# Kernel optimization log

Hardware: AMD Instinct MI355X
Metric: run time of the kernel (lower is better)

The kernel has to match this reference:

```python
import jax, jax.numpy as jnp
import numpy as np

D_MODEL, D_K, D_V, H = 512, 64, 64, 8
B, NQ, NK = 4, 2048, 2048


def setup_inputs() -> dict:
    key = jax.random.key(0)
    ks = jax.random.split(key, 14)
    s = 0.02
    return {
        "queries": jax.random.normal(ks[0], (B, NQ, D_MODEL), jnp.float32),
        "keys": jax.random.normal(ks[1], (B, NK, D_MODEL), jnp.float32),
        "values": jax.random.normal(ks[2], (B, NK, D_MODEL), jnp.float32),
        "attention_weights": jax.random.uniform(ks[3], (B, H, NQ, NK), jnp.float32),
        "attention_mask": jax.random.bernoulli(ks[4], 0.1, (B, H, NQ, NK)),
        "Wq": jax.random.normal(ks[5], (D_MODEL, H * D_K), jnp.float32) * s,
        "bq": jnp.zeros((H * D_K,), jnp.float32),
        "Wk": jax.random.normal(ks[6], (D_MODEL, H * D_K), jnp.float32) * s,
        "bk": jnp.zeros((H * D_K,), jnp.float32),
        "Wv": jax.random.normal(ks[7], (D_MODEL, H * D_V), jnp.float32) * s,
        "bv": jnp.zeros((H * D_V,), jnp.float32),
        "Wo": jax.random.normal(ks[8], (H * D_V, D_MODEL), jnp.float32) * s,
        "bo": jnp.zeros((D_MODEL,), jnp.float32),
    }


def reference(queries, keys, values, attention_weights, attention_mask,
              Wq, bq, Wk, bk, Wv, bv, Wo, bo):
    b_s, nq, _ = queries.shape
    nk = keys.shape[1]
    # projections -> (b, h, seq, d)
    q = (queries @ Wq + bq).reshape(b_s, nq, H, D_K).transpose(0, 2, 1, 3)
    k = (keys @ Wk + bk).reshape(b_s, nk, H, D_K).transpose(0, 2, 1, 3)
    v = (values @ Wv + bv).reshape(b_s, nk, H, D_V).transpose(0, 2, 1, 3)
    scale = 1.0 / np.sqrt(D_K).astype(np.float32)
    att = jnp.einsum("bhqd,bhkd->bhqk", q, k) * scale
    att = att * attention_weights
    att = jnp.where(attention_mask, -jnp.inf, att)
    att = jax.nn.softmax(att, axis=-1)
    out = jnp.einsum("bhqk,bhkd->bhqd", att, v)
    out = out.transpose(0, 2, 1, 3).reshape(b_s, nq, H * D_V)
    return out @ Wo + bo
```

## Files before the change

### kernel.cpp

```cpp
#include <hip/hip_runtime.h>
#include <hip/hip_bf16.h>
#include <math.h>

#define B_   4
#define H_   8
#define NQ_  2048
#define NK_  2048
#define DM_  512
#define DK_  64
#define WL_  262144

typedef short  bf16x8 __attribute__((ext_vector_type(8)));
typedef float  f32x4  __attribute__((ext_vector_type(4)));

static __device__ __forceinline__ f32x4 MFMA16(bf16x8 a, bf16x8 b, f32x4 c) {
    return __builtin_amdgcn_mfma_f32_16x16x32_bf16(a, b, c, 0, 0, 0);
}
static __device__ __forceinline__ unsigned short f2bf(float f) {
    __hip_bfloat16 h = __float2bfloat16(f);
    unsigned short u; __builtin_memcpy(&u, &h, 2); return u;
}
static __device__ __forceinline__ float bf2f(unsigned short u) {
    unsigned int x = ((unsigned int)u) << 16;
    float f; __builtin_memcpy(&f, &x, 4); return f;
}
static __device__ __forceinline__ void glds16(const void* g, void* l) {
    __builtin_amdgcn_global_load_lds(
        (__attribute__((address_space(1))) const void*)g,
        (__attribute__((address_space(3))) void*)l, 16, 0, 0);
}

__global__ __launch_bounds__(256) void conv_mask(const unsigned char* __restrict__ Mk,
                                                 unsigned long long* __restrict__ bits)
{
    __shared__ int s_flag;
    const int tid = threadIdx.x;
    if (tid == 0) s_flag = 0;
    __syncthreads();
    {
        bool any = false;
#pragma unroll
        for (int i = 1; i < 16; i += 4)
            if (Mk[tid*16 + i]) any = true;
        if (any) s_flag = 1;
    }
    __syncthreads();

    const long long NELEM = (long long)B_*H_*NQ_*NK_;
    const long long nth   = (long long)gridDim.x * 256;
    const long long T     = (long long)blockIdx.x * 256 + tid;
    unsigned short* b16   = (unsigned short*)bits;
    const uint4*    src   = (const uint4*)Mk;

    if (s_flag) {
        const long long n = NELEM / 16;
        for (long long t = T; t < n; t += nth) {
            const uint4 u = src[t];
            const unsigned int w[4] = {u.x, u.y, u.z, u.w};
            unsigned int m = 0;
#pragma unroll
            for (int j = 0; j < 4; ++j)
#pragma unroll
                for (int b2 = 0; b2 < 4; ++b2)
                    if ((w[j] >> (8*b2)) & 0xffu) m |= 1u << (4*j + b2);
            b16[t] = (unsigned short)m;
        }
    } else {
        const long long n = NELEM / 4;
        const int l3 = tid & 3;
        for (long long t = T; t < n; t += nth) {
            const uint4 u = src[t];
            const unsigned int nib = (u.x ? 1u : 0u) | (u.y ? 2u : 0u) |
                                     (u.z ? 4u : 0u) | (u.w ? 8u : 0u);
            unsigned int v = nib << (4*l3);
            v |= __shfl_xor(v, 1, 64);
            v |= __shfl_xor(v, 2, 64);
            if (l3 == 0) b16[t >> 2] = (unsigned short)v;
        }
    }
}

__global__ __launch_bounds__(256) void wprep(const float* __restrict__ Wq,
                                             const float* __restrict__ Wk,
                                             const float* __restrict__ Wv,
                                             const float* __restrict__ Wo,
                                             unsigned short* __restrict__ out)
{
    __shared__ float tile[64][65];
    const int tid = threadIdx.x;
    const int k0 = blockIdx.x * 64, n0 = blockIdx.y * 64, w = blockIdx.z;
    const float* W = (w == 0) ? Wq : (w == 1) ? Wk : (w == 2) ? Wv : Wo;
    unsigned short* WTh = out + (size_t)w * 2 * WL_;
    unsigned short* WTl = WTh + WL_;

#pragma unroll
    for (int rd = 0; rd < 4; ++rd) {
        const int k = (tid >> 4) + 16*rd, c4 = (tid & 15) * 4;
        const float4 v4 = *(const float4*)(W + (size_t)(k0 + k)*DM_ + n0 + c4);
        tile[k][c4+0] = v4.x; tile[k][c4+1] = v4.y;
        tile[k][c4+2] = v4.z; tile[k][c4+3] = v4.w;
    }
    __syncthreads();
#pragma unroll
    for (int rd = 0; rd < 4; ++rd) {
        const int n = (tid >> 4) + 16*rd, kk = (tid & 15) * 4;
        unsigned short hh[4], ll[4];
#pragma unroll
        for (int j = 0; j < 4; ++j) {
            const float f = tile[kk + j][n];
            hh[j] = f2bf(f);
            ll[j] = f2bf(f - bf2f(hh[j]));
        }
        *(ushort4*)(WTh + (size_t)(n0 + n)*DM_ + k0 + kk) = make_ushort4(hh[0],hh[1],hh[2],hh[3]);
        *(ushort4*)(WTl + (size_t)(n0 + n)*DM_ + k0 + kk) = make_ushort4(ll[0],ll[1],ll[2],ll[3]);
    }
}

template<int MODE>
__global__ __launch_bounds__(256) void gemm_split(
    const float* __restrict__ A,
    const unsigned short* __restrict__ WTh,
    const unsigned short* __restrict__ WTl,
    const float* __restrict__ bias,
    void* __restrict__ outv, const float oscale)
{
    __shared__ unsigned short Ah[64][64], Al[64][64], Bh[64][64], Bl[64][64];

    const int tid = threadIdx.x;
    const int w = tid >> 6, lane = tid & 63, g = lane >> 4, r = lane & 15;
    const int m0 = blockIdx.x * 64, n0 = blockIdx.y * 64;

    char* pAh = (char*)&Ah[0][0];
    char* pAl = (char*)&Al[0][0];
    char* pBh = (char*)&Bh[0][0];
    char* pBl = (char*)&Bl[0][0];

    const f32x4 z4 = {0.f, 0.f, 0.f, 0.f};
    f32x4 acc[4] = {z4, z4, z4, z4};

    for (int kt = 0; kt < DM_; kt += 64) {
#pragma unroll
        for (int rd = 0; rd < 4; ++rd) {
            const int row = (tid >> 4) + 16*rd;
            const int c4  = (tid & 15) * 4;
            const float4 a4 = *(const float4*)(A + (size_t)(m0 + row)*DM_ + kt + c4);
            const float av[4] = {a4.x, a4.y, a4.z, a4.w};
            unsigned short hh[4];
#pragma unroll
            for (int j = 0; j < 4; ++j) hh[j] = f2bf(av[j]);
            const int bo = (c4 * 2) ^ ((row & 7) << 4);
            *(ushort4*)(pAh + row*128 + bo) = make_ushort4(hh[0],hh[1],hh[2],hh[3]);
            if (MODE == 2) {
                unsigned short ll[4];
#pragma unroll
                for (int j = 0; j < 4; ++j) ll[j] = f2bf(av[j] - bf2f(hh[j]));
                *(ushort4*)(pAl + row*128 + bo) = make_ushort4(ll[0],ll[1],ll[2],ll[3]);
            }
        }
#pragma unroll
        for (int rd = 0; rd < 2; ++rd) {
            const int idx = tid + 256*rd;
            const int row = idx >> 3;
            const int cb  = (idx & 7) * 16;
            const int bo  = cb ^ ((row & 7) << 4);
            const size_t goff = (size_t)(n0 + row)*DM_ + kt + (cb >> 1);
            *(bf16x8*)(pBh + row*128 + bo) = *(const bf16x8*)(WTh + goff);
            *(bf16x8*)(pBl + row*128 + bo) = *(const bf16x8*)(WTl + goff);
        }
        __syncthreads();

        const int swr = (r & 7) << 4;
#pragma unroll
        for (int ks = 0; ks < 2; ++ks) {
            const int xo = (64*ks + 16*g) ^ swr;
            const bf16x8 xh = *(const bf16x8*)(pAh + (16*w + r)*128 + xo);
#pragma unroll
            for (int nt = 0; nt < 4; ++nt) {
                const bf16x8 bh = *(const bf16x8*)(pBh + (16*nt + r)*128 + xo);
                const bf16x8 bl = *(const bf16x8*)(pBl + (16*nt + r)*128 + xo);
                if (MODE == 1) {
                    acc[nt] = MFMA16(xh, bh, acc[nt]);
                    acc[nt] = MFMA16(xh, bl, acc[nt]);
                } else if (MODE == 0) {
                    acc[nt] = MFMA16(bh, xh, acc[nt]);
                    acc[nt] = MFMA16(bl, xh, acc[nt]);
                } else {
                    const bf16x8 xl = *(const bf16x8*)(pAl + (16*w + r)*128 + xo);
                    acc[nt] = MFMA16(bh, xh, acc[nt]);
                    acc[nt] = MFMA16(bh, xl, acc[nt]);
                    acc[nt] = MFMA16(bl, xh, acc[nt]);
                }
            }
        }
        __syncthreads();
    }

    if (MODE == 0) {
        const int m = m0 + 16*w + r;
        const int b = m >> 11, q = m & 2047, h = blockIdx.y;
        unsigned short* dst = (unsigned short*)outv + (((size_t)(b*H_ + h))*NQ_ + q)*DK_;
#pragma unroll
        for (int nt = 0; nt < 4; ++nt) {
            unsigned short u[4];
#pragma unroll
            for (int j = 0; j < 4; ++j)
                u[j] = f2bf((acc[nt][j] + bias[n0 + 16*nt + 4*g + j]) * oscale);
            *(ushort4*)(dst + 16*nt + 4*g) = make_ushort4(u[0],u[1],u[2],u[3]);
        }
    } else if (MODE == 1) {
        const int b = m0 >> 11, h = blockIdx.y;
        const int key = (m0 & 2047) + 16*w + 4*g;
#pragma unroll
        for (int nt = 0; nt < 4; ++nt) {
            const int dv = 16*nt + r;
            const float bv = bias[n0 + dv];
            unsigned short u[4];
#pragma unroll
            for (int j = 0; j < 4; ++j) u[j] = f2bf(acc[nt][j] + bv);
            *(ushort4*)((unsigned short*)outv +
                        (((size_t)(b*H_ + h))*DK_ + dv)*NK_ + key) = make_ushort4(u[0],u[1],u[2],u[3]);
        }
    } else {
        const int m = m0 + 16*w + r;
        float* dst = (float*)outv + (size_t)m*DM_ + n0;
#pragma unroll
        for (int nt = 0; nt < 4; ++nt) {
            float4 o4;
            o4.x = acc[nt][0] + bias[n0 + 16*nt + 4*g + 0];
            o4.y = acc[nt][1] + bias[n0 + 16*nt + 4*g + 1];
            o4.z = acc[nt][2] + bias[n0 + 16*nt + 4*g + 2];
            o4.w = acc[nt][3] + bias[n0 + 16*nt + 4*g + 3];
            *(float4*)(dst + 16*nt + 4*g) = o4;
        }
    }
}

__global__ __launch_bounds__(256, 2) void attn_mfma(
    const unsigned short* __restrict__ Qb,
    const unsigned short* __restrict__ Kb,
    const unsigned short* __restrict__ Vt,
    const float* __restrict__ Wt,
    const unsigned long long* __restrict__ Mb,
    float* __restrict__ O)
{
    __shared__ unsigned short KT[2][64][64];
    __shared__ unsigned short VTs[2][64][64];
    __shared__ float          WT[2][64][64];
    __shared__ short          Pl[4][1024];

    const int tid  = threadIdx.x;
    const int wv   = tid >> 6, lane = tid & 63;
    const int g    = lane >> 4, r = lane & 15;
    const int q0   = blockIdx.x * 64 + wv * 16;
    const int bh   = blockIdx.y;

    const size_t kvBase = (size_t)bh * NK_ * DK_;
    const unsigned short* qp = Qb + kvBase + (size_t)(q0 + r)*DK_ + 8*g;
    const bf16x8 qf0 = *(const bf16x8*)qp;
    const bf16x8 qf1 = *(const bf16x8*)(qp + 32);

    const float* wblock = Wt + ((size_t)bh*NQ_ + blockIdx.x*64)*NK_;
    const unsigned long long* brow = Mb + ((size_t)bh*NQ_ + q0 + r)*(NK_/64);
    const unsigned short* kg = Kb + kvBase;
    const unsigned short* vg = Vt + kvBase;

    const f32x4 zero4 = {0.f, 0.f, 0.f, 0.f};
    f32x4 oa0 = zero4, oa1 = zero4, oa2 = zero4, oa3 = zero4;
    float m_run = -1e30f, l_run = 0.f;

    char* pbase = (char*)&Pl[wv][0];
    const int roff = r * 128;
    const int sw   = (r & 7) << 4;

    const int kv_soff = 8 * ((lane & 7) ^ (lane >> 3));
    const int kv_r8   = lane >> 3;
    const int w_r4    = lane >> 4;

    auto stage = [&](int pbuf, int i) {
        const int kt = i * 64;
#pragma unroll
        for (int c = 0; c < 2; ++c) {
            const int rowl = 16*wv + c*8 + kv_r8;
            glds16(kg + (size_t)(kt + rowl)*DK_ + kv_soff,
                   &KT[pbuf][16*wv + c*8][0] + lane*8);
            glds16(vg + (size_t)rowl*NK_ + kt + kv_soff,
                   &VTs[pbuf][16*wv + c*8][0] + lane*8);
        }
#pragma unroll
        for (int c = 0; c < 4; ++c) {
            const int rowl = 16*wv + c*4 + w_r4;
            glds16(wblock + (size_t)rowl*NK_ + kt + 4*((lane & 15) ^ (c*4 + w_r4)),
                   &WT[pbuf][16*wv + c*4][0] + lane*4);
        }
    };

    stage(0, 0);
    __syncthreads();

#pragma unroll 1
    for (int i = 0; i < 32; ++i) {
        const int p = i & 1;

        if (i + 1 < 32) stage(p ^ 1, i + 1);
        const unsigned long long bcur = brow[i];

        f32x4 sa0 = zero4, sa1 = zero4, sa2 = zero4, sa3 = zero4;
        {
            const bf16x8 k00 = *(const bf16x8*)&KT[p][ 0 + r][8*((g    ) ^ (r & 7))];
            const bf16x8 k01 = *(const bf16x8*)&KT[p][ 0 + r][8*((g + 4) ^ (r & 7))];
            const bf16x8 k10 = *(const bf16x8*)&KT[p][16 + r][8*((g    ) ^ (r & 7))];
            const bf16x8 k11 = *(const bf16x8*)&KT[p][16 + r][8*((g + 4) ^ (r & 7))];
            const bf16x8 k20 = *(const bf16x8*)&KT[p][32 + r][8*((g    ) ^ (r & 7))];
            const bf16x8 k21 = *(const bf16x8*)&KT[p][32 + r][8*((g + 4) ^ (r & 7))];
            const bf16x8 k30 = *(const bf16x8*)&KT[p][48 + r][8*((g    ) ^ (r & 7))];
            const bf16x8 k31 = *(const bf16x8*)&KT[p][48 + r][8*((g + 4) ^ (r & 7))];
            sa0 = MFMA16(k00, qf0, sa0); sa0 = MFMA16(k01, qf1, sa0);
            sa1 = MFMA16(k10, qf0, sa1); sa1 = MFMA16(k11, qf1, sa1);
            sa2 = MFMA16(k20, qf0, sa2); sa2 = MFMA16(k21, qf1, sa2);
            sa3 = MFMA16(k30, qf0, sa3); sa3 = MFMA16(k31, qf1, sa3);
        }

        f32x4 wf[4];
#pragma unroll
        for (int t = 0; t < 4; ++t)
            wf[t] = *(const f32x4*)&WT[p][16*wv + r][4*((4*t + g) ^ r)];

        float lg[16];
        const f32x4 sav[4] = {sa0, sa1, sa2, sa3};
#pragma unroll
        for (int t = 0; t < 4; ++t) {
            const unsigned int half = (t & 2) ? (unsigned int)(bcur >> 32)
                                              : (unsigned int)bcur;
#pragma unroll
            for (int j = 0; j < 4; ++j) {
                const unsigned int bit = (half >> (16*(t & 1) + 4*g + j)) & 1u;
                lg[4*t+j] = bit ? -1e30f : sav[t][j] * wf[t][j];
            }
        }

        float mx = lg[0];
#pragma unroll
        for (int i2 = 1; i2 < 16; ++i2) mx = fmaxf(mx, lg[i2]);
        mx = fmaxf(mx, __shfl_xor(mx, 16, 64));
        mx = fmaxf(mx, __shfl_xor(mx, 32, 64));
        const float mnew = fmaxf(m_run, mx);
        const float fsc  = __expf(m_run - mnew);
        m_run = mnew;
        float p16[16], rs = 0.f;
#pragma unroll
        for (int i2 = 0; i2 < 16; ++i2) { p16[i2] = __expf(lg[i2] - mnew); rs += p16[i2]; }
        rs += __shfl_xor(rs, 16, 64);
        rs += __shfl_xor(rs, 32, 64);
        l_run = l_run * fsc + rs;

#pragma unroll
        for (int t = 0; t < 4; ++t) {
            const unsigned int w0 = (unsigned int)f2bf(p16[4*t+0]) |
                                    ((unsigned int)f2bf(p16[4*t+1]) << 16);
            const unsigned int w1 = (unsigned int)f2bf(p16[4*t+2]) |
                                    ((unsigned int)f2bf(p16[4*t+3]) << 16);
            *(int2*)(pbase + roff + ((32*t + 8*g) ^ sw)) = make_int2((int)w0, (int)w1);
        }
        const bf16x8 pa0 = *(const bf16x8*)(pbase + roff + ((     16*g) ^ sw));
        const bf16x8 pa1 = *(const bf16x8*)(pbase + roff + ((64 + 16*g) ^ sw));

        float fr[4];
#pragma unroll
        for (int j = 0; j < 4; ++j) fr[j] = __shfl(fsc, 4*g + j, 64);
#pragma unroll
        for (int j = 0; j < 4; ++j) {
            oa0[j] *= fr[j]; oa1[j] *= fr[j]; oa2[j] *= fr[j]; oa3[j] *= fr[j];
        }

        {
            const bf16x8 v00 = *(const bf16x8*)&VTs[p][ 0 + r][8*((g    ) ^ (r & 7))];
            const bf16x8 v01 = *(const bf16x8*)&VTs[p][16 + r][8*((g    ) ^ (r & 7))];
            const bf16x8 v02 = *(const bf16x8*)&VTs[p][32 + r][8*((g    ) ^ (r & 7))];
            const bf16x8 v03 = *(const bf16x8*)&VTs[p][48 + r][8*((g    ) ^ (r & 7))];
            const bf16x8 v10 = *(const bf16x8*)&VTs[p][ 0 + r][8*((g + 4) ^ (r & 7))];
            const bf16x8 v11 = *(const bf16x8*)&VTs[p][16 + r][8*((g + 4) ^ (r & 7))];
            const bf16x8 v12 = *(const bf16x8*)&VTs[p][32 + r][8*((g + 4) ^ (r & 7))];
            const bf16x8 v13 = *(const bf16x8*)&VTs[p][48 + r][8*((g + 4) ^ (r & 7))];
            oa0 = MFMA16(pa0, v00, oa0); oa1 = MFMA16(pa0, v01, oa1);
            oa2 = MFMA16(pa0, v02, oa2); oa3 = MFMA16(pa0, v03, oa3);
            oa0 = MFMA16(pa1, v10, oa0); oa1 = MFMA16(pa1, v11, oa1);
            oa2 = MFMA16(pa1, v12, oa2); oa3 = MFMA16(pa1, v13, oa3);
        }

        __syncthreads();
    }

    const float inv = 1.0f / l_run;
    float ir[4];
#pragma unroll
    for (int j = 0; j < 4; ++j) ir[j] = __shfl(inv, 4*g + j, 64);
    const int bb = bh >> 3, h = bh & 7;
    const f32x4 oav[4] = {oa0, oa1, oa2, oa3};
#pragma unroll
    for (int nt = 0; nt < 4; ++nt)
#pragma unroll
        for (int j = 0; j < 4; ++j)
            O[((size_t)(bb*NQ_ + q0 + 4*g + j))*DM_ + h*64 + 16*nt + r] = oav[nt][j] * ir[j];
}

extern "C" void kernel_launch(void* const* d_in, const int* in_sizes, int n_in,
                              void* d_out, int out_size, void* d_ws, size_t ws_size,
                              hipStream_t stream) {
    (void)in_sizes; (void)n_in; (void)out_size; (void)ws_size;

    const float* q    = (const float*)d_in[0];
    const float* k    = (const float*)d_in[1];
    const float* v    = (const float*)d_in[2];
    const float* attw = (const float*)d_in[3];
    const unsigned char* mask = (const unsigned char*)d_in[4];
    const float* Wq = (const float*)d_in[5];
    const float* bq = (const float*)d_in[6];
    const float* Wk = (const float*)d_in[7];
    const float* bk = (const float*)d_in[8];
    const float* Wv = (const float*)d_in[9];
    const float* bv = (const float*)d_in[10];
    const float* Wo = (const float*)d_in[11];
    const float* bo = (const float*)d_in[12];
    float* out = (float*)d_out;

    const long long NE = (long long)B_*H_*NQ_*DK_;
    unsigned short* q_bf = (unsigned short*)d_ws;
    unsigned short* k_bf = q_bf + NE;
    unsigned short* vT   = q_bf + 2*NE;
    unsigned short* wt   = q_bf + 3*NE;
    unsigned long long* bits = (unsigned long long*)(wt + 8LL*WL_);
    const long long NB = (long long)B_*H_*NQ_*NK_/64;
    float* o_ws = (float*)(bits + NB);

    const dim3 blk(256);
    wprep<<<dim3(8, 8, 4), blk, 0, stream>>>(Wq, Wk, Wv, Wo, wt);
    conv_mask<<<dim3(2048), blk, 0, stream>>>(mask, bits);

    const dim3 gg(128, 8);
    gemm_split<0><<<gg, blk, 0, stream>>>(q, wt + 0*WL_, wt + 1*WL_, bq, q_bf, 0.125f);
    gemm_split<0><<<gg, blk, 0, stream>>>(k, wt + 2*WL_, wt + 3*WL_, bk, k_bf, 1.0f);
    gemm_split<1><<<gg, blk, 0, stream>>>(v, wt + 4*WL_, wt + 5*WL_, bv, vT, 1.0f);

    attn_mfma<<<dim3(NQ_/64, B_*H_), blk, 0, stream>>>(q_bf, k_bf, vT, attw, bits, o_ws);

    gemm_split<2><<<gg, blk, 0, stream>>>(o_ws, wt + 6*WL_, wt + 7*WL_, bo, out, 1.0f);
}
```

Baseline: 405.0 us.

## Halve attention key tile to 32 and raise occupancy to four blocks per CU

The attention kernel now processes 32 keys per iteration instead of 64, which halves the shared-memory K/V/weight staging buffers and the per-thread register arrays. The launch bound is raised from 2 to 4 blocks per CU, and the mask is read as 32-bit words, with staging and swizzle patterns rewritten for the narrower tiles. The goal is more resident waves to hide memory latency on the attention-weight stream. The cost is twice as many loop iterations, online-softmax rescales and __syncthreads barriers, with less work per barrier.

```diff
diff --git a/kernel.cpp b/kernel.cpp
--- a/kernel.cpp
+++ b/kernel.cpp
@@ -235,17 +235,17 @@
     }
 }
 
-__global__ __launch_bounds__(256, 2) void attn_mfma(
+__global__ __launch_bounds__(256, 4) void attn_mfma(
     const unsigned short* __restrict__ Qb,
     const unsigned short* __restrict__ Kb,
     const unsigned short* __restrict__ Vt,
     const float* __restrict__ Wt,
-    const unsigned long long* __restrict__ Mb,
+    const unsigned int* __restrict__ Mb32,
     float* __restrict__ O)
 {
-    __shared__ unsigned short KT[2][64][64];
-    __shared__ unsigned short VTs[2][64][64];
-    __shared__ float          WT[2][64][64];
+    __shared__ unsigned short KT[2][32][64];
+    __shared__ unsigned short VTs[2][64][32];
+    __shared__ float          WT[2][64][32];
     __shared__ short          Pl[4][1024];
 
     const int tid  = threadIdx.x;
@@ -260,7 +260,7 @@
     const bf16x8 qf1 = *(const bf16x8*)(qp + 32);
 
     const float* wblock = Wt + ((size_t)bh*NQ_ + blockIdx.x*64)*NK_;
-    const unsigned long long* brow = Mb + ((size_t)bh*NQ_ + q0 + r)*(NK_/64);
+    const unsigned int* brow32 = Mb32 + ((size_t)bh*NQ_ + q0 + r)*(NK_/32);
     const unsigned short* kg = Kb + kvBase;
     const unsigned short* vg = Vt + kvBase;
 
@@ -272,97 +272,83 @@
     const int roff = r * 128;
     const int sw   = (r & 7) << 4;
 
-    const int kv_soff = 8 * ((lane & 7) ^ (lane >> 3));
-    const int kv_r8   = lane >> 3;
-    const int w_r4    = lane >> 4;
-
-    auto stage = [&](int pbuf, int i) {
-        const int kt = i * 64;
-#pragma unroll
-        for (int c = 0; c < 2; ++c) {
-            const int rowl = 16*wv + c*8 + kv_r8;
-            glds16(kg + (size_t)(kt + rowl)*DK_ + kv_soff,
-                   &KT[pbuf][16*wv + c*8][0] + lane*8);
-            glds16(vg + (size_t)rowl*NK_ + kt + kv_soff,
-                   &VTs[pbuf][16*wv + c*8][0] + lane*8);
-        }
-#pragma unroll
-        for (int c = 0; c < 4; ++c) {
-            const int rowl = 16*wv + c*4 + w_r4;
-            glds16(wblock + (size_t)rowl*NK_ + kt + 4*((lane & 15) ^ (c*4 + w_r4)),
-                   &WT[pbuf][16*wv + c*4][0] + lane*4);
-        }
+    const int l8  = lane >> 3;
+    const int c8  = lane & 7;
+    const int l4  = lane >> 2;
+    const int c4  = lane & 3;
+    const int kw_src = c8 ^ (l8 & 7);
+    const int v_src  = c4 ^ (l8 & 3);
+
+    auto stage = [&](int pbuf, int kt) {
+        glds16(kg + (size_t)(kt + 8*wv + l8)*DK_ + 8*kw_src,
+               &KT[pbuf][8*wv][0] + lane*8);
+        glds16(vg + (size_t)(16*wv + l4)*NK_ + kt + 8*v_src,
+               &VTs[pbuf][16*wv][0] + lane*8);
+#pragma unroll
+        for (int c = 0; c < 2; ++c)
+            glds16(wblock + (size_t)(16*wv + 8*c + l8)*NK_ + kt + 4*kw_src,
+                   &WT[pbuf][16*wv + 8*c][0] + lane*4);
     };
 
     stage(0, 0);
     __syncthreads();
 
 #pragma unroll 1
-    for (int i = 0; i < 32; ++i) {
+    for (int i = 0; i < 64; ++i) {
         const int p = i & 1;
 
-        if (i + 1 < 32) stage(p ^ 1, i + 1);
-        const unsigned long long bcur = brow[i];
-
-        f32x4 sa0 = zero4, sa1 = zero4, sa2 = zero4, sa3 = zero4;
+        if (i + 1 < 64) stage(p ^ 1, (i + 1) * 32);
+        const unsigned int bcur = brow32[i];
+
+        f32x4 sa0 = zero4, sa1 = zero4;
         {
             const bf16x8 k00 = *(const bf16x8*)&KT[p][ 0 + r][8*((g    ) ^ (r & 7))];
             const bf16x8 k01 = *(const bf16x8*)&KT[p][ 0 + r][8*((g + 4) ^ (r & 7))];
             const bf16x8 k10 = *(const bf16x8*)&KT[p][16 + r][8*((g    ) ^ (r & 7))];
             const bf16x8 k11 = *(const bf16x8*)&KT[p][16 + r][8*((g + 4) ^ (r & 7))];
-            const bf16x8 k20 = *(const bf16x8*)&KT[p][32 + r][8*((g    ) ^ (r & 7))];
-            const bf16x8 k21 = *(const bf16x8*)&KT[p][32 + r][8*((g + 4) ^ (r & 7))];
-            const bf16x8 k30 = *(const bf16x8*)&KT[p][48 + r][8*((g    ) ^ (r & 7))];
-            const bf16x8 k31 = *(const bf16x8*)&KT[p][48 + r][8*((g + 4) ^ (r & 7))];
             sa0 = MFMA16(k00, qf0, sa0); sa0 = MFMA16(k01, qf1, sa0);
             sa1 = MFMA16(k10, qf0, sa1); sa1 = MFMA16(k11, qf1, sa1);
-            sa2 = MFMA16(k20, qf0, sa2); sa2 = MFMA16(k21, qf1, sa2);
-            sa3 = MFMA16(k30, qf0, sa3); sa3 = MFMA16(k31, qf1, sa3);
-        }
-
-        f32x4 wf[4];
-#pragma unroll
-        for (int t = 0; t < 4; ++t)
-            wf[t] = *(const f32x4*)&WT[p][16*wv + r][4*((4*t + g) ^ r)];
-
-        float lg[16];
-        const f32x4 sav[4] = {sa0, sa1, sa2, sa3};
-#pragma unroll
-        for (int t = 0; t < 4; ++t) {
-            const unsigned int half = (t & 2) ? (unsigned int)(bcur >> 32)
-                                              : (unsigned int)bcur;
+        }
+
+        f32x4 wf[2];
+#pragma unroll
+        for (int t = 0; t < 2; ++t)
+            wf[t] = *(const f32x4*)&WT[p][16*wv + r][4*((4*t + g) ^ (r & 7))];
+
+        float lg[8];
+        const f32x4 sav[2] = {sa0, sa1};
+#pragma unroll
+        for (int t = 0; t < 2; ++t)
 #pragma unroll
             for (int j = 0; j < 4; ++j) {
-                const unsigned int bit = (half >> (16*(t & 1) + 4*g + j)) & 1u;
+                const unsigned int bit = (bcur >> (16*t + 4*g + j)) & 1u;
                 lg[4*t+j] = bit ? -1e30f : sav[t][j] * wf[t][j];
             }
-        }
 
         float mx = lg[0];
 #pragma unroll
-        for (int i2 = 1; i2 < 16; ++i2) mx = fmaxf(mx, lg[i2]);
+        for (int i2 = 1; i2 < 8; ++i2) mx = fmaxf(mx, lg[i2]);
         mx = fmaxf(mx, __shfl_xor(mx, 16, 64));
         mx = fmaxf(mx, __shfl_xor(mx, 32, 64));
         const float mnew = fmaxf(m_run, mx);
         const float fsc  = __expf(m_run - mnew);
         m_run = mnew;
-        float p16[16], rs = 0.f;
-#pragma unroll
-        for (int i2 = 0; i2 < 16; ++i2) { p16[i2] = __expf(lg[i2] - mnew); rs += p16[i2]; }
+        float p16[8], rs = 0.f;
+#pragma unroll
+        for (int i2 = 0; i2 < 8; ++i2) { p16[i2] = __expf(lg[i2] - mnew); rs += p16[i2]; }
         rs += __shfl_xor(rs, 16, 64);
         rs += __shfl_xor(rs, 32, 64);
         l_run = l_run * fsc + rs;
 
 #pragma unroll
-        for (int t = 0; t < 4; ++t) {
+        for (int t = 0; t < 2; ++t) {
             const unsigned int w0 = (unsigned int)f2bf(p16[4*t+0]) |
                                     ((unsigned int)f2bf(p16[4*t+1]) << 16);
             const unsigned int w1 = (unsigned int)f2bf(p16[4*t+2]) |
                                     ((unsigned int)f2bf(p16[4*t+3]) << 16);
             *(int2*)(pbase + roff + ((32*t + 8*g) ^ sw)) = make_int2((int)w0, (int)w1);
         }
-        const bf16x8 pa0 = *(const bf16x8*)(pbase + roff + ((     16*g) ^ sw));
-        const bf16x8 pa1 = *(const bf16x8*)(pbase + roff + ((64 + 16*g) ^ sw));
+        const bf16x8 pa = *(const bf16x8*)(pbase + roff + ((16*g) ^ sw));
 
         float fr[4];
 #pragma unroll
@@ -373,18 +359,13 @@
         }
 
         {
-            const bf16x8 v00 = *(const bf16x8*)&VTs[p][ 0 + r][8*((g    ) ^ (r & 7))];
-            const bf16x8 v01 = *(const bf16x8*)&VTs[p][16 + r][8*((g    ) ^ (r & 7))];
-            const bf16x8 v02 = *(const bf16x8*)&VTs[p][32 + r][8*((g    ) ^ (r & 7))];
-            const bf16x8 v03 = *(const bf16x8*)&VTs[p][48 + r][8*((g    ) ^ (r & 7))];
-            const bf16x8 v10 = *(const bf16x8*)&VTs[p][ 0 + r][8*((g + 4) ^ (r & 7))];
-            const bf16x8 v11 = *(const bf16x8*)&VTs[p][16 + r][8*((g + 4) ^ (r & 7))];
-            const bf16x8 v12 = *(const bf16x8*)&VTs[p][32 + r][8*((g + 4) ^ (r & 7))];
-            const bf16x8 v13 = *(const bf16x8*)&VTs[p][48 + r][8*((g + 4) ^ (r & 7))];
-            oa0 = MFMA16(pa0, v00, oa0); oa1 = MFMA16(pa0, v01, oa1);
-            oa2 = MFMA16(pa0, v02, oa2); oa3 = MFMA16(pa0, v03, oa3);
-            oa0 = MFMA16(pa1, v10, oa0); oa1 = MFMA16(pa1, v11, oa1);
-            oa2 = MFMA16(pa1, v12, oa2); oa3 = MFMA16(pa1, v13, oa3);
+            const int vc = 8*(g ^ ((r >> 1) & 3));
+            const bf16x8 v0 = *(const bf16x8*)&VTs[p][ 0 + r][vc];
+            const bf16x8 v1 = *(const bf16x8*)&VTs[p][16 + r][vc];
+            const bf16x8 v2 = *(const bf16x8*)&VTs[p][32 + r][vc];
+            const bf16x8 v3 = *(const bf16x8*)&VTs[p][48 + r][vc];
+            oa0 = MFMA16(pa, v0, oa0); oa1 = MFMA16(pa, v1, oa1);
+            oa2 = MFMA16(pa, v2, oa2); oa3 = MFMA16(pa, v3, oa3);
         }
 
         __syncthreads();
@@ -441,7 +422,8 @@
     gemm_split<0><<<gg, blk, 0, stream>>>(k, wt + 2*WL_, wt + 3*WL_, bk, k_bf, 1.0f);
     gemm_split<1><<<gg, blk, 0, stream>>>(v, wt + 4*WL_, wt + 5*WL_, bv, vT, 1.0f);
 
-    attn_mfma<<<dim3(NQ_/64, B_*H_), blk, 0, stream>>>(q_bf, k_bf, vT, attw, bits, o_ws);
+    attn_mfma<<<dim3(NQ_/64, B_*H_), blk, 0, stream>>>(q_bf, k_bf, vT, attw,
+                                                       (const unsigned int*)bits, o_ws);
 
     gemm_split<2><<<gg, blk, 0, stream>>>(o_ws, wt + 6*WL_, wt + 7*WL_, bo, out, 1.0f);
 }
```

Result: slower. 424.0 us (+4.7%).
